# Kernel tuning notes

Hardware: AMD Instinct MI355X
Metric: run time of the kernel (lower is better)

Reference implementation:

```python
import jax, jax.numpy as jnp
import numpy as np

B, H, S, D = 4, 16, 2048, 128

def setup_inputs() -> dict:
    key = jax.random.key(0)
    kk, kq, kv = jax.random.split(key, 3)
    k = jax.random.normal(kk, (B, H, S, D), dtype=jnp.float32)
    q = jax.random.normal(kq, (B, H, S, D), dtype=jnp.float32)
    v = jax.random.normal(kv, (B, H, S, D), dtype=jnp.float32)
    # causal mask: True = masked out (strictly upper triangle)
    mask = jnp.triu(jnp.ones((S, S), dtype=bool), k=1)
    return {"k": k, "q": q, "v": v, "mask": mask}

def reference(k, q, v, mask):
    d_k = k.shape[-1]
    # scores: [B, H, S, S]
    scores = jnp.einsum("bhqd,bhkd->bhqk", q, k) / jnp.sqrt(jnp.asarray(d_k, q.dtype))
    scores = jnp.where(mask, -jnp.inf, scores)
    # numerically stable softmax over last dim (matches manual max/exp/sum)
    p = jax.nn.softmax(scores, axis=-1)
    return jnp.einsum("bhqk,bhkd->bhqd", p, v)
```

## Files before the change

### kernel.cpp

```cpp
#include <hip/hip_runtime.h>
#include <hip/hip_bf16.h>
#include <math.h>

#define BATCH 4
#define HEADS 16
#define SEQ   2048
#define DIM   128
#define BHN   (BATCH*HEADS)

#define BQ 64
#define WQ 16
#define KT 32
#define NXB (SEQ/BQ)

typedef short bf16x8 __attribute__((ext_vector_type(8)));
typedef float f32x4  __attribute__((ext_vector_type(4)));

static __device__ __forceinline__ unsigned short f2bf(float f) {
    union { float f; unsigned u; } x; x.f = f;
    unsigned r = x.u + 0x7FFF + ((x.u >> 16) & 1);
    return (unsigned short)(r >> 16);
}

static __device__ __forceinline__ void async_cp16(const unsigned short* g, unsigned short* l) {
    __builtin_amdgcn_global_load_lds(
        (const __attribute__((address_space(1))) unsigned int*)g,
        (__attribute__((address_space(3))) unsigned int*)l,
        16, 0, 0);
}

__global__ __launch_bounds__(256) void cvt_kv(
    const float* __restrict__ k, const float* __restrict__ v,
    unsigned short* __restrict__ kb, unsigned short* __restrict__ vt) {
    const int bh = blockIdx.y;
    const int s0 = blockIdx.x * 64;
    const int t  = threadIdx.x;
    const long rbase = ((long)bh * SEQ + s0) * DIM;

    #pragma unroll
    for (int u = 0; u < 2; ++u) {
        long e = rbase + (long)(t + u * 256) * 16;
        const float* src = k + e;
        unsigned short* dst = kb + e;
        #pragma unroll
        for (int h = 0; h < 2; ++h) {
            float4 a0 = *(const float4*)(src + h * 8);
            float4 a1 = *(const float4*)(src + h * 8 + 4);
            union { uint4 q; __hip_bfloat162 b[4]; } p;
            p.b[0] = __float22bfloat162_rn(float2{a0.x, a0.y});
            p.b[1] = __float22bfloat162_rn(float2{a0.z, a0.w});
            p.b[2] = __float22bfloat162_rn(float2{a1.x, a1.y});
            p.b[3] = __float22bfloat162_rn(float2{a1.z, a1.w});
            *(uint4*)(dst + h * 8) = p.q;
        }
    }
    {
        const int rg = t & 15;
        const int dg = t >> 4;
        const float* src = v + rbase + (long)(rg * 4) * DIM + dg * 8;
        float a[4][8];
        #pragma unroll
        for (int rr = 0; rr < 4; ++rr) {
            float4 x = *(const float4*)(src + rr * DIM);
            float4 y = *(const float4*)(src + rr * DIM + 4);
            a[rr][0]=x.x; a[rr][1]=x.y; a[rr][2]=x.z; a[rr][3]=x.w;
            a[rr][4]=y.x; a[rr][5]=y.y; a[rr][6]=y.z; a[rr][7]=y.w;
        }
        unsigned short* dstb = vt + ((long)bh * DIM + dg * 8) * SEQ + s0 + rg * 4;
        #pragma unroll
        for (int dd = 0; dd < 8; ++dd) {
            union { uint2 u; __hip_bfloat162 b[2]; } p;
            p.b[0] = __float22bfloat162_rn(float2{a[0][dd], a[1][dd]});
            p.b[1] = __float22bfloat162_rn(float2{a[2][dd], a[3][dd]});
            *(uint2*)(dstb + (long)dd * SEQ) = p.u;
        }
    }
}

__global__ __launch_bounds__(256, 4) void attn_fwd(
    const float* __restrict__ qg,
    const unsigned short* __restrict__ kb,
    const unsigned short* __restrict__ vtg,
    float* __restrict__ out) {

    __shared__ unsigned short Kt[2][KT][DIM];
    __shared__ unsigned short Vt[2][DIM][KT];
    __shared__ unsigned short Pl[4][16][KT + 8];

    const int tid  = threadIdx.x;
    const int w    = tid >> 6;
    const int lane = tid & 63;
    const int quad = lane >> 4;
    const int ql   = lane & 15;

    const int flat = blockIdx.x;
    const int xcd  = flat & 7;
    const int slot = flat >> 3;
    const int bh   = (xcd << 3) | (slot & 7);
    const int shi  = slot >> 3;
    const int c_   = shi & 3;
    const int j_   = shi >> 2;
    const int xb   = (j_ & 1) ? (28 + c_ - 4 * j_) : (31 - c_ - 4 * j_);
    const int qb0 = xb * BQ;
    const int qw0 = qb0 + w * WQ;

    const long base = (long)bh * SEQ * DIM;
    const float scale = 0.08838834764831845f * 1.4426950408889634f;

    bf16x8 qf[4];
    {
        const float* qr = qg + base + (long)(qw0 + ql) * DIM;
        #pragma unroll
        for (int c = 0; c < 4; ++c) {
            const float* p = qr + c * 32 + quad * 8;
            float4 x = *(const float4*)(p);
            float4 y = *(const float4*)(p + 4);
            union { bf16x8 v; unsigned short s[8]; } u;
            u.s[0]=f2bf(x.x*scale); u.s[1]=f2bf(x.y*scale);
            u.s[2]=f2bf(x.z*scale); u.s[3]=f2bf(x.w*scale);
            u.s[4]=f2bf(y.x*scale); u.s[5]=f2bf(y.y*scale);
            u.s[6]=f2bf(y.z*scale); u.s[7]=f2bf(y.w*scale);
            qf[c] = u.v;
        }
    }

    f32x4 acc[8];
    #pragma unroll
    for (int n = 0; n < 8; ++n) acc[n] = (f32x4){0.f, 0.f, 0.f, 0.f};

    float m_ = -INFINITY;
    float l_ = 0.f;

    int koff[2], voff[2];
    #pragma unroll
    for (int i = 0; i < 2; ++i) {
        const int idx = tid + i * 256;
        const int r   = idx >> 4;
        const int chg = (idx & 15) ^ (r & 15);
        koff[i] = r * DIM + chg * 8;
        const int d   = idx >> 2;
        const int cvg = (idx & 3) ^ ((d >> 1) & 3);
        voff[i] = d * SEQ + cvg * 8;
    }
    const int ldso = ((tid >> 6) * 64) * 8;
    const unsigned short* kbb = kb + base;
    const unsigned short* vbb = vtg + base;

    auto stage = [&](int buf, int k0s) {
        const unsigned short* ku = kbb + k0s * DIM;
        const unsigned short* vu = vbb + k0s;
        #pragma unroll
        for (int i = 0; i < 2; ++i) {
            async_cp16(ku + koff[i], &Kt[buf][0][0] + ldso + i * 2048);
            async_cp16(vu + voff[i], &Vt[buf][0][0] + ldso + i * 2048);
        }
    };

    const unsigned short* kfb[4];
    #pragma unroll
    for (int c = 0; c < 4; ++c)
        kfb[c] = &Kt[0][ql][((c * 4 + quad) ^ ql) * 8];
    const unsigned short* vfb = &Vt[0][0][0] + ql * KT + (quad ^ ((ql >> 1) & 3)) * 8;
    unsigned short* pwb = &Pl[w][ql][0];
    const unsigned short* prb = &Pl[w][ql][quad * 8];

    auto body = [&](const int buf, const int k0) {
        if (k0 >= qw0 + WQ) return;
        const int kbo = buf * (KT * DIM);
        const int vbo = buf * (DIM * KT);

        f32x4 sacc0 = (f32x4){0.f, 0.f, 0.f, 0.f};
        f32x4 sacc1 = (f32x4){0.f, 0.f, 0.f, 0.f};
        __builtin_amdgcn_s_setprio(1);
        #pragma unroll
        for (int c = 0; c < 4; ++c) {
            bf16x8 kf0 = *(const bf16x8*)(kfb[c] + kbo);
            bf16x8 kf1 = *(const bf16x8*)(kfb[c] + kbo + 16 * DIM);
            sacc0 = __builtin_amdgcn_mfma_f32_16x16x32_bf16(kf0, qf[c], sacc0, 0, 0, 0);
            sacc1 = __builtin_amdgcn_mfma_f32_16x16x32_bf16(kf1, qf[c], sacc1, 0, 0, 0);
        }
        __builtin_amdgcn_s_setprio(0);

        bf16x8 vf[8];
        #pragma unroll
        for (int n = 0; n < 8; ++n)
            vf[n] = *(const bf16x8*)(vfb + vbo + n * (16 * KT));

        const int qrow   = qw0 + ql;
        const bool needm = (k0 + KT - 1 > qw0);
        float s[2][4];
        float tmax = -INFINITY;
        #pragma unroll
        for (int kk = 0; kk < 2; ++kk)
            #pragma unroll
            for (int r = 0; r < 4; ++r) {
                float sv = (kk ? sacc1 : sacc0)[r];
                if (needm) {
                    int kg = k0 + kk * 16 + quad * 4 + r;
                    sv = (kg <= qrow) ? sv : -INFINITY;
                }
                s[kk][r] = sv;
                tmax = fmaxf(tmax, sv);
            }
        tmax = fmaxf(tmax, __shfl_xor(tmax, 16));
        tmax = fmaxf(tmax, __shfl_xor(tmax, 32));

        const bool skip = __all(tmax <= m_ + 4.0f);
        const float mnew = skip ? m_ : fmaxf(m_, tmax);

        float rsum = 0.f;
        #pragma unroll
        for (int kk = 0; kk < 2; ++kk) {
            float p0 = __builtin_amdgcn_exp2f(s[kk][0] - mnew);
            float p1 = __builtin_amdgcn_exp2f(s[kk][1] - mnew);
            float p2 = __builtin_amdgcn_exp2f(s[kk][2] - mnew);
            float p3 = __builtin_amdgcn_exp2f(s[kk][3] - mnew);
            rsum += (p0 + p1) + (p2 + p3);
            union { uint2 u; __hip_bfloat162 h[2]; } pu;
            pu.h[0] = __float22bfloat162_rn(float2{p0, p1});
            pu.h[1] = __float22bfloat162_rn(float2{p2, p3});
            *(uint2*)(pwb + kk * 16 + quad * 4) = pu.u;
        }
        rsum += __shfl_xor(rsum, 16);
        rsum += __shfl_xor(rsum, 32);

        float alpha;
        bool  resc;
        if (skip) {
            l_ += rsum;
            alpha = 1.f; resc = false;
        } else {
            alpha = __builtin_amdgcn_exp2f(m_ - mnew);
            l_ = l_ * alpha + rsum;
            m_ = mnew;
            resc = true;
        }

        if (resc) {
            #pragma unroll
            for (int r = 0; r < 4; ++r) {
                float ar = __shfl(alpha, quad * 4 + r);
                #pragma unroll
                for (int n = 0; n < 8; ++n) acc[n][r] *= ar;
            }
        }

        bf16x8 pf = *(const bf16x8*)prb;
        __builtin_amdgcn_s_setprio(1);
        #pragma unroll
        for (int n = 0; n < 8; ++n)
            acc[n] = __builtin_amdgcn_mfma_f32_16x16x32_bf16(pf, vf[n], acc[n], 0, 0, 0);
        __builtin_amdgcn_s_setprio(0);
    };

    const int ntile = 2 * xb + 2;

    stage(0, 0);

    for (int tt = 0; tt < ntile; tt += 2) {
        __syncthreads();
        if (tt + 1 < ntile) stage(1, (tt + 1) * KT);
        body(0, tt * KT);

        __syncthreads();
        if (tt + 2 < ntile) stage(0, (tt + 2) * KT);
        body(1, (tt + 1) * KT);
    }

    #pragma unroll
    for (int r = 0; r < 4; ++r) {
        float lr = __shfl(l_, quad * 4 + r);
        float il = 1.0f / lr;
        long orow = base + (long)(qw0 + quad * 4 + r) * DIM;
        #pragma unroll
        for (int n = 0; n < 8; ++n)
            out[orow + n * 16 + ql] = acc[n][r] * il;
    }
}

extern "C" void kernel_launch(void* const* d_in, const int* in_sizes, int n_in,
                              void* d_out, int out_size, void* d_ws, size_t ws_size,
                              hipStream_t stream) {
    const float* k = (const float*)d_in[0];
    const float* q = (const float*)d_in[1];
    const float* v = (const float*)d_in[2];
    float* o = (float*)d_out;

    unsigned short* kb = (unsigned short*)d_ws;
    unsigned short* vt = kb + (size_t)BHN * SEQ * DIM;

    cvt_kv<<<dim3(SEQ / 64, BHN), dim3(256), 0, stream>>>(k, v, kb, vt);

    attn_fwd<<<dim3(NXB * BHN), dim3(256), 0, stream>>>(q, kb, vt, o);
}
```

Before: 321.8 us.

## Keep softmax probabilities in registers using 16x16x16 MFMA for PV

Drops the per-wave LDS staging buffer for P. The S accumulator fragments are converted to bf16 and fed straight into two 16x16x16 bf16 MFMAs per output tile, whose operand layout matches the accumulator layout. To match, the V LDS swizzle and the fragment reads are rearranged into 4-element halves. This removes an LDS write/read round trip per tile, at the cost of issuing twice as many, smaller MFMAs for PV. The change also raises the launch-bounds occupancy target to 5 blocks, which risks register pressure, and makes the second-buffer staging unconditional.

After: 473.5 us. +47.1%, slower.

```diff
diff --git a/kernel.cpp b/kernel.cpp
--- a/kernel.cpp
+++ b/kernel.cpp
@@ -14,12 +14,24 @@
 #define NXB (SEQ/BQ)
 
 typedef short bf16x8 __attribute__((ext_vector_type(8)));
+typedef short bf16x4 __attribute__((ext_vector_type(4)));
 typedef float f32x4  __attribute__((ext_vector_type(4)));
 
 static __device__ __forceinline__ unsigned short f2bf(float f) {
     union { float f; unsigned u; } x; x.f = f;
     unsigned r = x.u + 0x7FFF + ((x.u >> 16) & 1);
     return (unsigned short)(r >> 16);
+}
+
+static __device__ __forceinline__ f32x4 mfma16(bf16x4 a, bf16x4 b, f32x4 c) {
+#if __has_builtin(__builtin_amdgcn_mfma_f32_16x16x16bf16_1k)
+    return __builtin_amdgcn_mfma_f32_16x16x16bf16_1k(a, b, c, 0, 0, 0);
+#else
+    f32x4 d;
+    asm("v_mfma_f32_16x16x16_bf16 %0, %1, %2, %3"
+        : "=v"(d) : "v"(a), "v"(b), "v"(c));
+    return d;
+#endif
 }
 
 static __device__ __forceinline__ void async_cp16(const unsigned short* g, unsigned short* l) {
@@ -77,7 +89,7 @@
     }
 }
 
-__global__ __launch_bounds__(256, 4) void attn_fwd(
+__global__ __launch_bounds__(256, 5) void attn_fwd(
     const float* __restrict__ qg,
     const unsigned short* __restrict__ kb,
     const unsigned short* __restrict__ vtg,
@@ -85,7 +97,6 @@
 
     __shared__ unsigned short Kt[2][KT][DIM];
     __shared__ unsigned short Vt[2][DIM][KT];
-    __shared__ unsigned short Pl[4][16][KT + 8];
 
     const int tid  = threadIdx.x;
     const int w    = tid >> 6;
@@ -139,7 +150,7 @@
         const int chg = (idx & 15) ^ (r & 15);
         koff[i] = r * DIM + chg * 8;
         const int d   = idx >> 2;
-        const int cvg = (idx & 3) ^ ((d >> 1) & 3);
+        const int cvg = (idx & 3) ^ (d & 3);
         voff[i] = d * SEQ + cvg * 8;
     }
     const int ldso = ((tid >> 6) * 64) * 8;
@@ -160,9 +171,9 @@
     #pragma unroll
     for (int c = 0; c < 4; ++c)
         kfb[c] = &Kt[0][ql][((c * 4 + quad) ^ ql) * 8];
-    const unsigned short* vfb = &Vt[0][0][0] + ql * KT + (quad ^ ((ql >> 1) & 3)) * 8;
-    unsigned short* pwb = &Pl[w][ql][0];
-    const unsigned short* prb = &Pl[w][ql][quad * 8];
+    const unsigned short* vfb = &Vt[0][0][0] + ql * KT;
+    const int vswz0 = ((quad)     ^ (2 * (ql & 3))) * 4;
+    const int vswz1 = ((4 + quad) ^ (2 * (ql & 3))) * 4;
 
     auto body = [&](const int buf, const int k0) {
         if (k0 >= qw0 + WQ) return;
@@ -181,10 +192,12 @@
         }
         __builtin_amdgcn_s_setprio(0);
 
-        bf16x8 vf[8];
-        #pragma unroll
-        for (int n = 0; n < 8; ++n)
-            vf[n] = *(const bf16x8*)(vfb + vbo + n * (16 * KT));
+        bf16x4 vf0[8], vf1[8];
+        #pragma unroll
+        for (int n = 0; n < 8; ++n) {
+            vf0[n] = *(const bf16x4*)(vfb + vbo + n * (16 * KT) + vswz0);
+            vf1[n] = *(const bf16x4*)(vfb + vbo + n * (16 * KT) + vswz1);
+        }
 
         const int qrow   = qw0 + ql;
         const bool needm = (k0 + KT - 1 > qw0);
@@ -209,6 +222,7 @@
         const float mnew = skip ? m_ : fmaxf(m_, tmax);
 
         float rsum = 0.f;
+        bf16x4 pf0, pf1;
         #pragma unroll
         for (int kk = 0; kk < 2; ++kk) {
             float p0 = __builtin_amdgcn_exp2f(s[kk][0] - mnew);
@@ -216,10 +230,10 @@
             float p2 = __builtin_amdgcn_exp2f(s[kk][2] - mnew);
             float p3 = __builtin_amdgcn_exp2f(s[kk][3] - mnew);
             rsum += (p0 + p1) + (p2 + p3);
-            union { uint2 u; __hip_bfloat162 h[2]; } pu;
+            union { bf16x4 v; __hip_bfloat162 h[2]; } pu;
             pu.h[0] = __float22bfloat162_rn(float2{p0, p1});
             pu.h[1] = __float22bfloat162_rn(float2{p2, p3});
-            *(uint2*)(pwb + kk * 16 + quad * 4) = pu.u;
+            if (kk == 0) pf0 = pu.v; else pf1 = pu.v;
         }
         rsum += __shfl_xor(rsum, 16);
         rsum += __shfl_xor(rsum, 32);
@@ -245,11 +259,12 @@
             }
         }
 
-        bf16x8 pf = *(const bf16x8*)prb;
         __builtin_amdgcn_s_setprio(1);
         #pragma unroll
-        for (int n = 0; n < 8; ++n)
-            acc[n] = __builtin_amdgcn_mfma_f32_16x16x32_bf16(pf, vf[n], acc[n], 0, 0, 0);
+        for (int n = 0; n < 8; ++n) {
+            acc[n] = mfma16(pf0, vf0[n], acc[n]);
+            acc[n] = mfma16(pf1, vf1[n], acc[n]);
+        }
         __builtin_amdgcn_s_setprio(0);
     };
 
@@ -259,7 +274,7 @@
 
     for (int tt = 0; tt < ntile; tt += 2) {
         __syncthreads();
-        if (tt + 1 < ntile) stage(1, (tt + 1) * KT);
+        stage(1, (tt + 1) * KT);
         body(0, tt * KT);
 
         __syncthreads();
```
